# Optimization experiments

Measured on AMD Instinct MI355X. Metric: run time of the kernel, lower is better.

Reference implementation:

```python
import jax, jax.numpy as jnp
import numpy as np

T, B, D = 200, 2048, 256
H1, H2, H3 = 512, 256, 1
LABEL_LEN = 10


def _linear_init(key, fan_in, fan_out):
    lim = 1.0 / np.sqrt(fan_in)
    kw, kb = jax.random.split(key)
    W = jax.random.uniform(kw, (fan_in, fan_out), minval=-lim, maxval=lim, dtype=jnp.float32)
    b = jax.random.uniform(kb, (fan_out,), minval=-lim, maxval=lim, dtype=jnp.float32)
    return W, b


def setup_inputs() -> dict:
    key = jax.random.key(0)
    ks = jax.random.split(key, 8)
    inputs = jax.random.normal(ks[0], (T, B, D), dtype=jnp.float32)  # padded, time-major [T,B,D]
    lengths = jnp.sort(jax.random.randint(ks[1], (B,), LABEL_LEN, T + 1))[::-1]
    lengths = lengths.at[0].set(T)  # packed-seq: descending lengths, max = T
    ctr_W1, ctr_b1 = _linear_init(ks[2], D, H1)
    ctr_W2, ctr_b2 = _linear_init(ks[3], H1, H2)
    ctr_W3, ctr_b3 = _linear_init(ks[4], H2, H3)
    cvr_W1, cvr_b1 = _linear_init(ks[5], D, H1)
    cvr_W2, cvr_b2 = _linear_init(ks[6], H1, H2)
    cvr_W3, cvr_b3 = _linear_init(ks[7], H2, H3)
    return dict(inputs=inputs, lengths=lengths, label_len=LABEL_LEN,
                ctr_W1=ctr_W1, ctr_b1=ctr_b1, ctr_W2=ctr_W2, ctr_b2=ctr_b2,
                ctr_W3=ctr_W3, ctr_b3=ctr_b3,
                cvr_W1=cvr_W1, cvr_b1=cvr_b1, cvr_W2=cvr_W2, cvr_b2=cvr_b2,
                cvr_W3=cvr_W3, cvr_b3=cvr_b3)


def _tower(x, W1, b1, W2, b2, W3, b3):
    # Dropout is identity in eval; LeakyReLU slope 0.01 (torch default).
    x = jax.nn.leaky_relu(x @ W1 + b1)
    x = jax.nn.leaky_relu(x @ W2 + b2)
    x = jax.nn.leaky_relu(x @ W3 + b3)
    return x


def reference(inputs, lengths, label_len,
              ctr_W1, ctr_b1, ctr_W2, ctr_b2, ctr_W3, ctr_b3,
              cvr_W1, cvr_b1, cvr_W2, cvr_b2, cvr_W3, cvr_b3):
    # f1: O(T) prefix-sum replaces the original O(T^2) per-step torch.mean loop.
    cs = jnp.cumsum(inputs, axis=0)                              # [T,B,D]
    # h[j,k] = mean over prefix of length L_j - label_len + k + 1
    idx = lengths[:, None] - label_len + jnp.arange(label_len)   # [B,label_len], time index
    cs_bt = cs.transpose(1, 0, 2)                                # [B,T,D]
    h = jnp.take_along_axis(cs_bt, idx[:, :, None], axis=1)      # [B,label_len,D]
    h = h / (idx[:, :, None] + 1).astype(inputs.dtype)
    h_ctr = jax.nn.sigmoid(_tower(h, ctr_W1, ctr_b1, ctr_W2, ctr_b2, ctr_W3, ctr_b3))
    h_cvr = jax.nn.sigmoid(_tower(h, cvr_W1, cvr_b1, cvr_W2, cvr_b2, cvr_W3, cvr_b3))
    return h_ctr * h_cvr                                         # [B,label_len,1]
```

## Files before the change

kernel.cpp:

```cpp
#include <hip/hip_runtime.h>
#include <math.h>

#define B_DIM 2048
#define D_DIM 256
#define H1 512
#define H2 256
#define LBL 10
#define M_ROWS (B_DIM * LBL)
#define LD_A1 520
#define WSZ1 (H1 * D_DIM)
#define WSZ2 (H2 * H1)

typedef __attribute__((ext_vector_type(8))) short frag_ab;
typedef __attribute__((ext_vector_type(4))) float frag_cd;

__device__ __forceinline__ float leaky(float v) { return v > 0.f ? v : 0.01f * v; }

__device__ __forceinline__ unsigned short f2bf(float f) {
  union { float f; unsigned int u; } v;
  v.f = f;
  unsigned int r = v.u + 0x7FFFu + ((v.u >> 16) & 1u);
  return (unsigned short)(r >> 16);
}

__device__ __forceinline__ void acc4(float4& s, const float4 a) {
  s.x += a.x; s.y += a.y; s.z += a.z; s.w += a.w;
}

__global__ __launch_bounds__(256) void prologue_kernel(
    const float* __restrict__ x, const int* __restrict__ lens,
    unsigned short* __restrict__ hb,
    const float* __restrict__ W1a, const float* __restrict__ W1b,
    const float* __restrict__ W2a, const float* __restrict__ W2b,
    unsigned short* __restrict__ P1, unsigned short* __restrict__ P2) {
  __shared__ float4 partial[4][64];
  const int bx = blockIdx.x;
  const int tid = threadIdx.x;

  if (bx < 128) {
    const int tw = bx >> 6;
    const int idx = (bx & 63) * 256 + tid;
    const float* __restrict__ in = tw ? W1b : W1a;
    const int l = idx & 63;
    const int n = (idx >> 6) & 15;
    const int ks = (idx >> 10) & 7;
    const int cbh = idx >> 13;
    const int col = cbh * 256 + n * 16 + (l & 15);
    const int k0 = ks * 32 + (l >> 4) * 8;
    unsigned short o[8];
    #pragma unroll
    for (int jj = 0; jj < 8; ++jj)
      o[jj] = f2bf(in[(size_t)(k0 + jj) * H1 + col]);
    ushort4* dst = reinterpret_cast<ushort4*>(P1 + (size_t)tw * WSZ1 + (size_t)idx * 8);
    dst[0] = make_ushort4(o[0], o[1], o[2], o[3]);
    dst[1] = make_ushort4(o[4], o[5], o[6], o[7]);
    return;
  }
  if (bx < 256) {
    const int pb = bx - 128;
    const int tw = pb >> 6;
    const int idx = (pb & 63) * 256 + tid;
    const float* __restrict__ in = tw ? W2b : W2a;
    const int l = idx & 63;
    const int n = (idx >> 6) & 7;
    const int ks = (idx >> 9) & 15;
    const int cbh = idx >> 13;
    const int col = cbh * 128 + n * 16 + (l & 15);
    const int k0 = ks * 32 + (l >> 4) * 8;
    unsigned short o[8];
    #pragma unroll
    for (int jj = 0; jj < 8; ++jj)
      o[jj] = f2bf(in[(size_t)(k0 + jj) * H2 + col]);
    ushort4* dst = reinterpret_cast<ushort4*>(P2 + (size_t)tw * WSZ2 + (size_t)idx * 8);
    dst[0] = make_ushort4(o[0], o[1], o[2], o[3]);
    dst[1] = make_ushort4(o[4], o[5], o[6], o[7]);
    return;
  }

  const int wv = tid >> 6;
  const int lane = tid & 63;
  const int bid = bx - 256;
  const int b = (bid & 1) ? (B_DIM - 1 - (bid >> 1)) : (bid >> 1);
  const int L = lens[b];
  const int Lm = L - LBL;
  const size_t ts = (size_t)(B_DIM * D_DIM / 4);
  const float4* xb = reinterpret_cast<const float4*>(x) + (size_t)b * (D_DIM / 4) + lane;
  const int c0 = (Lm * wv) >> 2;
  const int c1 = (wv == 3) ? Lm : ((Lm * (wv + 1)) >> 2);
  float4 s0 = make_float4(0.f, 0.f, 0.f, 0.f), s1 = s0, s2 = s0, s3 = s0;
  int t = c0;
  for (; t + 8 <= c1; t += 8) {
    float4 a0 = xb[(size_t)(t + 0) * ts], a1 = xb[(size_t)(t + 1) * ts];
    float4 a2 = xb[(size_t)(t + 2) * ts], a3 = xb[(size_t)(t + 3) * ts];
    float4 a4 = xb[(size_t)(t + 4) * ts], a5 = xb[(size_t)(t + 5) * ts];
    float4 a6 = xb[(size_t)(t + 6) * ts], a7 = xb[(size_t)(t + 7) * ts];
    acc4(s0, a0); acc4(s1, a1); acc4(s2, a2); acc4(s3, a3);
    acc4(s0, a4); acc4(s1, a5); acc4(s2, a6); acc4(s3, a7);
  }
  for (; t < c1; ++t) acc4(s0, xb[(size_t)t * ts]);
  acc4(s0, s1); acc4(s2, s3); acc4(s0, s2);
  partial[wv][lane] = s0;
  __syncthreads();
  if (wv == 3) {
    float4 s = partial[0][lane];
    acc4(s, partial[1][lane]);
    acc4(s, partial[2][lane]);
    acc4(s, partial[3][lane]);
    #pragma unroll
    for (int k = 0; k < LBL; ++k) {
      const int tt = Lm + k;
      acc4(s, xb[(size_t)tt * ts]);
      const float inv = 1.0f / (float)(tt + 1);
      ushort4 o;
      o.x = f2bf(s.x * inv); o.y = f2bf(s.y * inv);
      o.z = f2bf(s.z * inv); o.w = f2bf(s.w * inv);
      *reinterpret_cast<ushort4*>(hb + (size_t)(b * LBL + k) * D_DIM + lane * 4) = o;
    }
  }
}

__global__ __launch_bounds__(256, 4) void tower_mfma(
    const unsigned short* __restrict__ hb,
    const unsigned short* __restrict__ P1,
    const unsigned short* __restrict__ P2,
    const float* __restrict__ b1a, const float* __restrict__ b2a,
    const float* __restrict__ w3a, const float* __restrict__ b3a,
    const float* __restrict__ b1b, const float* __restrict__ b2b,
    const float* __restrict__ w3b, const float* __restrict__ b3b,
    float* __restrict__ sigbuf) {
  __shared__ unsigned short A1[32][LD_A1];
  __shared__ float part[2][32];
  const int tid = threadIdx.x;
  const int l = tid & 63;
  const int w = tid >> 6;
  const int lr = l & 15;
  const int lg = l >> 4;
  const int rb = (w & 1) * 16;
  const int cbh = w >> 1;
  const int r0 = blockIdx.x * 32;
  const int tw = blockIdx.y;

  const unsigned short* __restrict__ pb1 =
      P1 + (size_t)tw * WSZ1 + (size_t)cbh * (WSZ1 / 2) + (size_t)l * 8;
  const unsigned short* __restrict__ pb2 =
      P2 + (size_t)tw * WSZ2 + (size_t)cbh * (WSZ2 / 2) + (size_t)l * 8;
  const float* __restrict__ B1 = tw ? b1b : b1a;
  const float* __restrict__ B2 = tw ? b2b : b2a;
  const float* __restrict__ W3 = tw ? w3b : w3a;
  const float* __restrict__ B3 = tw ? b3b : b3a;

  frag_cd acc1[16];
  #pragma unroll
  for (int n = 0; n < 16; ++n) {
    const float bv = B1[cbh * 256 + n * 16 + lr];
    acc1[n] = (frag_cd){bv, bv, bv, bv};
  }
  const unsigned short* arow = hb + (size_t)(r0 + rb + lr) * D_DIM;
  #pragma unroll
  for (int ks = 0; ks < D_DIM / 32; ++ks) {
    const frag_ab af = *reinterpret_cast<const frag_ab*>(arow + ks * 32 + lg * 8);
    #pragma unroll
    for (int n = 0; n < 16; ++n) {
      const frag_ab bf =
          *reinterpret_cast<const frag_ab*>(pb1 + (size_t)(ks * 16 + n) * 512);
      acc1[n] = __builtin_amdgcn_mfma_f32_16x16x32_bf16(af, bf, acc1[n], 0, 0, 0);
    }
  }
  #pragma unroll
  for (int n = 0; n < 16; ++n)
    #pragma unroll
    for (int r = 0; r < 4; ++r)
      A1[rb + lg * 4 + r][cbh * 256 + n * 16 + lr] = f2bf(leaky(acc1[n][r]));
  __syncthreads();

  frag_cd acc2[8];
  #pragma unroll
  for (int n = 0; n < 8; ++n) {
    const float bv = B2[cbh * 128 + n * 16 + lr];
    acc2[n] = (frag_cd){bv, bv, bv, bv};
  }
  #pragma unroll
  for (int ks = 0; ks < H1 / 32; ++ks) {
    const frag_ab af = *reinterpret_cast<const frag_ab*>(&A1[rb + lr][ks * 32 + lg * 8]);
    #pragma unroll
    for (int n = 0; n < 8; ++n) {
      const frag_ab bf =
          *reinterpret_cast<const frag_ab*>(pb2 + (size_t)(ks * 8 + n) * 512);
      acc2[n] = __builtin_amdgcn_mfma_f32_16x16x32_bf16(af, bf, acc2[n], 0, 0, 0);
    }
  }

  float s[4] = {0.f, 0.f, 0.f, 0.f};
  #pragma unroll
  for (int n = 0; n < 8; ++n) {
    const float w3v = W3[cbh * 128 + n * 16 + lr];
    #pragma unroll
    for (int r = 0; r < 4; ++r)
      s[r] = fmaf(leaky(acc2[n][r]), w3v, s[r]);
  }
  #pragma unroll
  for (int r = 0; r < 4; ++r) {
    s[r] += __shfl_xor(s[r], 1);
    s[r] += __shfl_xor(s[r], 2);
    s[r] += __shfl_xor(s[r], 4);
    s[r] += __shfl_xor(s[r], 8);
  }
  if (lr == 0) {
    #pragma unroll
    for (int r = 0; r < 4; ++r) part[cbh][rb + lg * 4 + r] = s[r];
  }
  __syncthreads();
  if (tid < 32) {
    const float z = leaky(part[0][tid] + part[1][tid] + B3[0]);
    sigbuf[(size_t)tw * M_ROWS + r0 + tid] = 1.f / (1.f + expf(-z));
  }
}

__global__ __launch_bounds__(256) void combine_kernel(
    const float* __restrict__ sigbuf, float* __restrict__ out) {
  const int i = blockIdx.x * 256 + threadIdx.x;
  out[i] = sigbuf[i] * sigbuf[M_ROWS + i];
}

extern "C" void kernel_launch(void* const* d_in, const int* in_sizes, int n_in,
                              void* d_out, int out_size, void* d_ws, size_t ws_size,
                              hipStream_t stream) {
  (void)in_sizes; (void)n_in; (void)out_size; (void)ws_size;
  const float* x    = (const float*)d_in[0];
  const int*   lens = (const int*)d_in[1];
  const float* cW1 = (const float*)d_in[3];
  const float* cb1 = (const float*)d_in[4];
  const float* cW2 = (const float*)d_in[5];
  const float* cb2 = (const float*)d_in[6];
  const float* cW3 = (const float*)d_in[7];
  const float* cb3 = (const float*)d_in[8];
  const float* vW1 = (const float*)d_in[9];
  const float* vb1 = (const float*)d_in[10];
  const float* vW2 = (const float*)d_in[11];
  const float* vb2 = (const float*)d_in[12];
  const float* vW3 = (const float*)d_in[13];
  const float* vb3 = (const float*)d_in[14];
  float* out = (float*)d_out;

  unsigned short* hb = (unsigned short*)d_ws;
  unsigned short* p1 = hb + (size_t)M_ROWS * D_DIM;
  unsigned short* p2 = p1 + 2 * WSZ1;
  float* sigbuf = (float*)(p2 + 2 * WSZ2);

  prologue_kernel<<<256 + B_DIM, 256, 0, stream>>>(
      x, lens, hb, cW1, vW1, cW2, vW2, p1, p2);
  tower_mfma<<<dim3(M_ROWS / 32, 2), 256, 0, stream>>>(
      hb, p1, p2, cb1, cb2, cW3, cb3, vb1, vb2, vW3, vb3, sigbuf);
  combine_kernel<<<M_ROWS / 256, 256, 0, stream>>>(sigbuf, out);
}
```

Before: 101.7 us.

## Fuse both towers and combine into one kernel; one wave per batch prefix sum

The tower kernel now loops over both towers inside each block and multiplies the two sigmoids in registers, writing the final output directly. This removes the separate combine kernel and the sigbuf round trip. The prologue now assigns one wave per batch row for the prefix sum instead of splitting one row across four waves with a shared-memory reduction, which shrinks the grid from 2304 to 768 blocks. The tower grid is halved, leaving 640 blocks doing twice the serial work each, so there is less parallelism. Each wave also runs a longer serial chain over up to 190 timesteps.

```diff
diff --git a/kernel.cpp b/kernel.cpp
--- a/kernel.cpp
+++ b/kernel.cpp
@@ -33,13 +33,47 @@
     const float* __restrict__ W1a, const float* __restrict__ W1b,
     const float* __restrict__ W2a, const float* __restrict__ W2b,
     unsigned short* __restrict__ P1, unsigned short* __restrict__ P2) {
-  __shared__ float4 partial[4][64];
   const int bx = blockIdx.x;
   const int tid = threadIdx.x;
 
-  if (bx < 128) {
-    const int tw = bx >> 6;
-    const int idx = (bx & 63) * 256 + tid;
+  if (bx < 512) {
+    const int wv = tid >> 6;
+    const int lane = tid & 63;
+    const int idx = bx * 4 + wv;
+    const int b = (idx & 1) ? (B_DIM - 1 - (idx >> 1)) : (idx >> 1);
+    const int L = lens[b];
+    const int Lm = L - LBL;
+    const size_t ts = (size_t)(B_DIM * D_DIM / 4);
+    const float4* xb =
+        reinterpret_cast<const float4*>(x) + (size_t)b * (D_DIM / 4) + lane;
+    float4 s0 = make_float4(0.f, 0.f, 0.f, 0.f), s1 = s0, s2 = s0, s3 = s0;
+    int t = 0;
+    for (; t + 8 <= Lm; t += 8) {
+      float4 a0 = xb[(size_t)(t + 0) * ts], a1 = xb[(size_t)(t + 1) * ts];
+      float4 a2 = xb[(size_t)(t + 2) * ts], a3 = xb[(size_t)(t + 3) * ts];
+      float4 a4 = xb[(size_t)(t + 4) * ts], a5 = xb[(size_t)(t + 5) * ts];
+      float4 a6 = xb[(size_t)(t + 6) * ts], a7 = xb[(size_t)(t + 7) * ts];
+      acc4(s0, a0); acc4(s1, a1); acc4(s2, a2); acc4(s3, a3);
+      acc4(s0, a4); acc4(s1, a5); acc4(s2, a6); acc4(s3, a7);
+    }
+    for (; t < Lm; ++t) acc4(s0, xb[(size_t)t * ts]);
+    acc4(s0, s1); acc4(s2, s3); acc4(s0, s2);
+    #pragma unroll
+    for (int k = 0; k < LBL; ++k) {
+      const int tt = Lm + k;
+      acc4(s0, xb[(size_t)tt * ts]);
+      const float inv = 1.0f / (float)(tt + 1);
+      ushort4 o;
+      o.x = f2bf(s0.x * inv); o.y = f2bf(s0.y * inv);
+      o.z = f2bf(s0.z * inv); o.w = f2bf(s0.w * inv);
+      *reinterpret_cast<ushort4*>(hb + (size_t)(b * LBL + k) * D_DIM + lane * 4) = o;
+    }
+    return;
+  }
+  if (bx < 640) {
+    const int pb = bx - 512;
+    const int tw = pb >> 6;
+    const int idx = (pb & 63) * 256 + tid;
     const float* __restrict__ in = tw ? W1b : W1a;
     const int l = idx & 63;
     const int n = (idx >> 6) & 15;
@@ -56,8 +90,8 @@
     dst[1] = make_ushort4(o[4], o[5], o[6], o[7]);
     return;
   }
-  if (bx < 256) {
-    const int pb = bx - 128;
+  {
+    const int pb = bx - 640;
     const int tw = pb >> 6;
     const int idx = (pb & 63) * 256 + tid;
     const float* __restrict__ in = tw ? W2b : W2a;
@@ -74,48 +108,6 @@
     ushort4* dst = reinterpret_cast<ushort4*>(P2 + (size_t)tw * WSZ2 + (size_t)idx * 8);
     dst[0] = make_ushort4(o[0], o[1], o[2], o[3]);
     dst[1] = make_ushort4(o[4], o[5], o[6], o[7]);
-    return;
-  }
-
-  const int wv = tid >> 6;
-  const int lane = tid & 63;
-  const int bid = bx - 256;
-  const int b = (bid & 1) ? (B_DIM - 1 - (bid >> 1)) : (bid >> 1);
-  const int L = lens[b];
-  const int Lm = L - LBL;
-  const size_t ts = (size_t)(B_DIM * D_DIM / 4);
-  const float4* xb = reinterpret_cast<const float4*>(x) + (size_t)b * (D_DIM / 4) + lane;
-  const int c0 = (Lm * wv) >> 2;
-  const int c1 = (wv == 3) ? Lm : ((Lm * (wv + 1)) >> 2);
-  float4 s0 = make_float4(0.f, 0.f, 0.f, 0.f), s1 = s0, s2 = s0, s3 = s0;
-  int t = c0;
-  for (; t + 8 <= c1; t += 8) {
-    float4 a0 = xb[(size_t)(t + 0) * ts], a1 = xb[(size_t)(t + 1) * ts];
-    float4 a2 = xb[(size_t)(t + 2) * ts], a3 = xb[(size_t)(t + 3) * ts];
-    float4 a4 = xb[(size_t)(t + 4) * ts], a5 = xb[(size_t)(t + 5) * ts];
-    float4 a6 = xb[(size_t)(t + 6) * ts], a7 = xb[(size_t)(t + 7) * ts];
-    acc4(s0, a0); acc4(s1, a1); acc4(s2, a2); acc4(s3, a3);
-    acc4(s0, a4); acc4(s1, a5); acc4(s2, a6); acc4(s3, a7);
-  }
-  for (; t < c1; ++t) acc4(s0, xb[(size_t)t * ts]);
-  acc4(s0, s1); acc4(s2, s3); acc4(s0, s2);
-  partial[wv][lane] = s0;
-  __syncthreads();
-  if (wv == 3) {
-    float4 s = partial[0][lane];
-    acc4(s, partial[1][lane]);
-    acc4(s, partial[2][lane]);
-    acc4(s, partial[3][lane]);
-    #pragma unroll
-    for (int k = 0; k < LBL; ++k) {
-      const int tt = Lm + k;
-      acc4(s, xb[(size_t)tt * ts]);
-      const float inv = 1.0f / (float)(tt + 1);
-      ushort4 o;
-      o.x = f2bf(s.x * inv); o.y = f2bf(s.y * inv);
-      o.z = f2bf(s.z * inv); o.w = f2bf(s.w * inv);
-      *reinterpret_cast<ushort4*>(hb + (size_t)(b * LBL + k) * D_DIM + lane * 4) = o;
-    }
   }
 }
 
@@ -127,7 +119,7 @@
     const float* __restrict__ w3a, const float* __restrict__ b3a,
     const float* __restrict__ b1b, const float* __restrict__ b2b,
     const float* __restrict__ w3b, const float* __restrict__ b3b,
-    float* __restrict__ sigbuf) {
+    float* __restrict__ out) {
   __shared__ unsigned short A1[32][LD_A1];
   __shared__ float part[2][32];
   const int tid = threadIdx.x;
@@ -138,88 +130,90 @@
   const int rb = (w & 1) * 16;
   const int cbh = w >> 1;
   const int r0 = blockIdx.x * 32;
-  const int tw = blockIdx.y;
-
-  const unsigned short* __restrict__ pb1 =
-      P1 + (size_t)tw * WSZ1 + (size_t)cbh * (WSZ1 / 2) + (size_t)l * 8;
-  const unsigned short* __restrict__ pb2 =
-      P2 + (size_t)tw * WSZ2 + (size_t)cbh * (WSZ2 / 2) + (size_t)l * 8;
-  const float* __restrict__ B1 = tw ? b1b : b1a;
-  const float* __restrict__ B2 = tw ? b2b : b2a;
-  const float* __restrict__ W3 = tw ? w3b : w3a;
-  const float* __restrict__ B3 = tw ? b3b : b3a;
-
-  frag_cd acc1[16];
-  #pragma unroll
-  for (int n = 0; n < 16; ++n) {
-    const float bv = B1[cbh * 256 + n * 16 + lr];
-    acc1[n] = (frag_cd){bv, bv, bv, bv};
-  }
-  const unsigned short* arow = hb + (size_t)(r0 + rb + lr) * D_DIM;
-  #pragma unroll
-  for (int ks = 0; ks < D_DIM / 32; ++ks) {
-    const frag_ab af = *reinterpret_cast<const frag_ab*>(arow + ks * 32 + lg * 8);
+
+  float prod = 0.f;
+
+  for (int tw = 0; tw < 2; ++tw) {
+    const unsigned short* __restrict__ pb1 =
+        P1 + (size_t)tw * WSZ1 + (size_t)cbh * (WSZ1 / 2) + (size_t)l * 8;
+    const unsigned short* __restrict__ pb2 =
+        P2 + (size_t)tw * WSZ2 + (size_t)cbh * (WSZ2 / 2) + (size_t)l * 8;
+    const float* __restrict__ B1 = tw ? b1b : b1a;
+    const float* __restrict__ B2 = tw ? b2b : b2a;
+    const float* __restrict__ W3 = tw ? w3b : w3a;
+    const float* __restrict__ B3 = tw ? b3b : b3a;
+
+    frag_cd acc1[16];
     #pragma unroll
     for (int n = 0; n < 16; ++n) {
-      const frag_ab bf =
-          *reinterpret_cast<const frag_ab*>(pb1 + (size_t)(ks * 16 + n) * 512);
-      acc1[n] = __builtin_amdgcn_mfma_f32_16x16x32_bf16(af, bf, acc1[n], 0, 0, 0);
-    }
-  }
-  #pragma unroll
-  for (int n = 0; n < 16; ++n)
-    #pragma unroll
-    for (int r = 0; r < 4; ++r)
-      A1[rb + lg * 4 + r][cbh * 256 + n * 16 + lr] = f2bf(leaky(acc1[n][r]));
-  __syncthreads();
-
-  frag_cd acc2[8];
-  #pragma unroll
-  for (int n = 0; n < 8; ++n) {
-    const float bv = B2[cbh * 128 + n * 16 + lr];
-    acc2[n] = (frag_cd){bv, bv, bv, bv};
-  }
-  #pragma unroll
-  for (int ks = 0; ks < H1 / 32; ++ks) {
-    const frag_ab af = *reinterpret_cast<const frag_ab*>(&A1[rb + lr][ks * 32 + lg * 8]);
+      const float bv = B1[cbh * 256 + n * 16 + lr];
+      acc1[n] = (frag_cd){bv, bv, bv, bv};
+    }
+    const unsigned short* arow = hb + (size_t)(r0 + rb + lr) * D_DIM;
+    #pragma unroll
+    for (int ks = 0; ks < D_DIM / 32; ++ks) {
+      const frag_ab af = *reinterpret_cast<const frag_ab*>(arow + ks * 32 + lg * 8);
+      #pragma unroll
+      for (int n = 0; n < 16; ++n) {
+        const frag_ab bf =
+            *reinterpret_cast<const frag_ab*>(pb1 + (size_t)(ks * 16 + n) * 512);
+        acc1[n] = __builtin_amdgcn_mfma_f32_16x16x32_bf16(af, bf, acc1[n], 0, 0, 0);
+      }
+    }
+    #pragma unroll
+    for (int n = 0; n < 16; ++n)
+      #pragma unroll
+      for (int r = 0; r < 4; ++r)
+        A1[rb + lg * 4 + r][cbh * 256 + n * 16 + lr] = f2bf(leaky(acc1[n][r]));
+    __syncthreads();
+
+    frag_cd acc2[8];
     #pragma unroll
     for (int n = 0; n < 8; ++n) {
-      const frag_ab bf =
-          *reinterpret_cast<const frag_ab*>(pb2 + (size_t)(ks * 8 + n) * 512);
-      acc2[n] = __builtin_amdgcn_mfma_f32_16x16x32_bf16(af, bf, acc2[n], 0, 0, 0);
-    }
-  }
-
-  float s[4] = {0.f, 0.f, 0.f, 0.f};
-  #pragma unroll
-  for (int n = 0; n < 8; ++n) {
-    const float w3v = W3[cbh * 128 + n * 16 + lr];
-    #pragma unroll
-    for (int r = 0; r < 4; ++r)
-      s[r] = fmaf(leaky(acc2[n][r]), w3v, s[r]);
-  }
-  #pragma unroll
-  for (int r = 0; r < 4; ++r) {
-    s[r] += __shfl_xor(s[r], 1);
-    s[r] += __shfl_xor(s[r], 2);
-    s[r] += __shfl_xor(s[r], 4);
-    s[r] += __shfl_xor(s[r], 8);
-  }
-  if (lr == 0) {
-    #pragma unroll
-    for (int r = 0; r < 4; ++r) part[cbh][rb + lg * 4 + r] = s[r];
-  }
-  __syncthreads();
-  if (tid < 32) {
-    const float z = leaky(part[0][tid] + part[1][tid] + B3[0]);
-    sigbuf[(size_t)tw * M_ROWS + r0 + tid] = 1.f / (1.f + expf(-z));
-  }
-}
-
-__global__ __launch_bounds__(256) void combine_kernel(
-    const float* __restrict__ sigbuf, float* __restrict__ out) {
-  const int i = blockIdx.x * 256 + threadIdx.x;
-  out[i] = sigbuf[i] * sigbuf[M_ROWS + i];
+      const float bv = B2[cbh * 128 + n * 16 + lr];
+      acc2[n] = (frag_cd){bv, bv, bv, bv};
+    }
+    #pragma unroll
+    for (int ks = 0; ks < H1 / 32; ++ks) {
+      const frag_ab af =
+          *reinterpret_cast<const frag_ab*>(&A1[rb + lr][ks * 32 + lg * 8]);
+      #pragma unroll
+      for (int n = 0; n < 8; ++n) {
+        const frag_ab bf =
+            *reinterpret_cast<const frag_ab*>(pb2 + (size_t)(ks * 8 + n) * 512);
+        acc2[n] = __builtin_amdgcn_mfma_f32_16x16x32_bf16(af, bf, acc2[n], 0, 0, 0);
+      }
+    }
+
+    float s[4] = {0.f, 0.f, 0.f, 0.f};
+    #pragma unroll
+    for (int n = 0; n < 8; ++n) {
+      const float w3v = W3[cbh * 128 + n * 16 + lr];
+      #pragma unroll
+      for (int r = 0; r < 4; ++r)
+        s[r] = fmaf(leaky(acc2[n][r]), w3v, s[r]);
+    }
+    #pragma unroll
+    for (int r = 0; r < 4; ++r) {
+      s[r] += __shfl_xor(s[r], 1);
+      s[r] += __shfl_xor(s[r], 2);
+      s[r] += __shfl_xor(s[r], 4);
+      s[r] += __shfl_xor(s[r], 8);
+    }
+    if (lr == 0) {
+      #pragma unroll
+      for (int r = 0; r < 4; ++r) part[cbh][rb + lg * 4 + r] = s[r];
+    }
+    __syncthreads();
+    if (tid < 32) {
+      const float z = leaky(part[0][tid] + part[1][tid] + B3[0]);
+      const float sg = 1.f / (1.f + expf(-z));
+      prod = tw ? prod * sg : sg;
+    }
+    __syncthreads();
+  }
+
+  if (tid < 32) out[r0 + tid] = prod;
 }
 
 extern "C" void kernel_launch(void* const* d_in, const int* in_sizes, int n_in,
@@ -245,11 +239,9 @@
   unsigned short* hb = (unsigned short*)d_ws;
   unsigned short* p1 = hb + (size_t)M_ROWS * D_DIM;
   unsigned short* p2 = p1 + 2 * WSZ1;
-  float* sigbuf = (float*)(p2 + 2 * WSZ2);
-
-  prologue_kernel<<<256 + B_DIM, 256, 0, stream>>>(
+
+  prologue_kernel<<<768, 256, 0, stream>>>(
       x, lens, hb, cW1, vW1, cW2, vW2, p1, p2);
-  tower_mfma<<<dim3(M_ROWS / 32, 2), 256, 0, stream>>>(
-      hb, p1, p2, cb1, cb2, cW3, cb3, vb1, vb2, vW3, vb3, sigbuf);
-  combine_kernel<<<M_ROWS / 256, 256, 0, stream>>>(sigbuf, out);
-}
+  tower_mfma<<<640, 256, 0, stream>>>(
+      hb, p1, p2, cb1, cb2, cW3, cb3, vb1, vb2, vW3, vb3, out);
+}
```

New measurement: 179.4 us. 1.76x slower.
